# Optimization experiments

Hardware: AMD Instinct MI355X
Metric: run time of the kernel (lower is better)

## Reference

```python
import jax, jax.numpy as jnp
import numpy as np

HEADS = 4
OUT_DIM = 64
NEG_SLOPE = 0.2


def setup_inputs() -> dict:
    key = jax.random.key(0)
    k1, k2, k3, k4 = jax.random.split(key, 4)
    n, in_dim = 4096, 256
    x = jax.random.normal(k1, (n, in_dim), dtype=jnp.float32)
    adj = jax.random.randint(k2, (n, n), 0, 2, dtype=jnp.int32)
    # lin: in_dim -> heads*out_dim (no bias), stored as [in_dim, heads*out_dim]
    W = jax.random.normal(k3, (in_dim, HEADS * OUT_DIM), dtype=jnp.float32) * 0.05
    # att_weight: [heads, 2*out_dim]
    att = jax.random.normal(k4, (HEADS, 2 * OUT_DIM), dtype=jnp.float32) * 0.05
    return {"x": x, "adj": adj, "W": W, "att": att}


def reference(x, adj, W, att):
    n = x.shape[0]
    h = (x @ W).reshape(n, HEADS, OUT_DIM)  # [n, H, D]
    # scores[i,j,h] = att[h] . cat(h_i, h_j) = <h_i, a_src[h]> + <h_j, a_dst[h]>
    a_src, a_dst = att[:, :OUT_DIM], att[:, OUT_DIM:]
    e_src = jnp.einsum('nhd,hd->nh', h, a_src)  # [n, H]
    e_dst = jnp.einsum('nhd,hd->nh', h, a_dst)  # [n, H]
    scores = e_src[:, None, :] + e_dst[None, :, :]  # [n, n, H]
    scores = jax.nn.leaky_relu(scores, negative_slope=NEG_SLOPE)
    mask = (adj > 0)[:, :, None]  # [n, n, 1]
    scores = jnp.where(mask, scores, -jnp.inf)
    alpha = jax.nn.softmax(scores, axis=1)  # softmax over neighbors j
    # h_prime[i,h,d] = sum_j alpha[i,j,h] * h[j,h,d]
    h_prime = jnp.einsum('ijh,jhd->ihd', alpha, h)
    return h_prime.reshape(n, HEADS * OUT_DIM)
```

## Files before the change

kernel.cpp:

```cpp
#include <hip/hip_runtime.h>
#include <hip/hip_bf16.h>

#define HEADS 4
#define ODIM 64
#define HD 256
#define NEG_SLOPE 0.2f

typedef __attribute__((ext_vector_type(8))) short bf16x8;
typedef __attribute__((ext_vector_type(4))) float floatx4;

__global__ __launch_bounds__(256) void pack_x(const float* __restrict__ x,
                                              __hip_bfloat16* __restrict__ xh,
                                              __hip_bfloat16* __restrict__ xl, int K) {
    const int g = blockIdx.x * 256 + threadIdx.x;
    const int lane = g & 63, frag = g >> 6;
    const int Kc = K >> 5;
    const int kc = frag % Kc, mc = frag / Kc;
    const int l16 = lane & 15, q = lane >> 4;
    const float* src = x + (size_t)(mc * 16 + l16) * K + kc * 32 + q * 8;
    const float4 v0 = *(const float4*)src;
    const float4 v1 = *(const float4*)(src + 4);
    const float vv[8] = {v0.x, v0.y, v0.z, v0.w, v1.x, v1.y, v1.z, v1.w};
    union { __hip_bfloat16 b[8]; bf16x8 v; } H, L;
    #pragma unroll
    for (int p = 0; p < 8; ++p) {
        H.b[p] = __float2bfloat16(vv[p]);
        L.b[p] = __float2bfloat16(vv[p] - __bfloat162float(H.b[p]));
    }
    *(bf16x8*)&xh[(size_t)frag * 512 + lane * 8] = H.v;
    *(bf16x8*)&xl[(size_t)frag * 512 + lane * 8] = L.v;
}

__global__ __launch_bounds__(256) void pack_w(const float* __restrict__ W,
                                              __hip_bfloat16* __restrict__ wh,
                                              __hip_bfloat16* __restrict__ wl,
                                              int N, int K) {
    const int g = blockIdx.x * 256 + threadIdx.x;
    const int lane = g & 63, frag = g >> 6;
    const int Kc = K >> 5;
    const int kc = frag % Kc, nc = frag / Kc;
    const int l16 = lane & 15, q = lane >> 4;
    union { __hip_bfloat16 b[8]; bf16x8 v; } H, L;
    #pragma unroll
    for (int p = 0; p < 8; ++p) {
        const float w = W[(size_t)(kc * 32 + q * 8 + p) * N + nc * 16 + l16];
        H.b[p] = __float2bfloat16(w);
        L.b[p] = __float2bfloat16(w - __bfloat162float(H.b[p]));
    }
    *(bf16x8*)&wh[(size_t)frag * 512 + lane * 8] = H.v;
    *(bf16x8*)&wl[(size_t)frag * 512 + lane * 8] = L.v;
}

__global__ __launch_bounds__(256) void gemm_fused(
    const __hip_bfloat16* __restrict__ xh, const __hip_bfloat16* __restrict__ xl,
    const __hip_bfloat16* __restrict__ wh, const __hip_bfloat16* __restrict__ wl,
    const float* __restrict__ att, float4* __restrict__ E4,
    __hip_bfloat16* __restrict__ hbB, int n, int K) {

    __shared__ __hip_bfloat16 T[64][80];

    const int tid = threadIdx.x, wave = tid >> 6, lane = tid & 63;
    const int q = lane >> 4, l16 = lane & 15;
    const int m0 = blockIdx.x * 64;
    const int head = blockIdx.y;
    const int Kc = K >> 5;
    const int mc = (m0 >> 4) + wave;

    floatx4 acc[4] = {{0.f,0.f,0.f,0.f},{0.f,0.f,0.f,0.f},{0.f,0.f,0.f,0.f},{0.f,0.f,0.f,0.f}};

    const __hip_bfloat16* Ab[3] = {xh, xh, xl};
    const __hip_bfloat16* Bb[3] = {wh, wl, wh};
    #pragma unroll
    for (int pass = 0; pass < 3; ++pass) {
        const __hip_bfloat16* A = Ab[pass] + (size_t)mc * Kc * 512 + lane * 8;
        const __hip_bfloat16* B = Bb[pass] + lane * 8;
        for (int kc = 0; kc < Kc; ++kc) {
            const bf16x8 af = *(const bf16x8*)(A + (size_t)kc * 512);
            #pragma unroll
            for (int nt = 0; nt < 4; ++nt) {
                const bf16x8 bf = *(const bf16x8*)(B + (size_t)((head * 4 + nt) * Kc + kc) * 512);
                acc[nt] = __builtin_amdgcn_mfma_f32_16x16x32_bf16(af, bf, acc[nt], 0, 0, 0);
            }
        }
    }

    float as_v[4], ad_v[4];
    #pragma unroll
    for (int nt = 0; nt < 4; ++nt) {
        as_v[nt] = att[head * 2 * ODIM + nt * 16 + l16];
        ad_v[nt] = att[head * 2 * ODIM + ODIM + nt * 16 + l16];
    }
    #pragma unroll
    for (int r = 0; r < 4; ++r) {
        float ps = 0.f, pd = 0.f;
        #pragma unroll
        for (int nt = 0; nt < 4; ++nt) {
            ps = fmaf(acc[nt][r], as_v[nt], ps);
            pd = fmaf(acc[nt][r], ad_v[nt], pd);
        }
        #pragma unroll
        for (int m = 1; m <= 8; m <<= 1) {
            ps += __shfl_xor(ps, m, 64);
            pd += __shfl_xor(pd, m, 64);
        }
        if (l16 == 0) {
            const int i = m0 + wave * 16 + q * 4 + r;
            E4[i * HEADS + head] = make_float4(__expf(ps), __expf(NEG_SLOPE * ps),
                                               __expf(pd), __expf(NEG_SLOPE * pd));
        }
    }

    #pragma unroll
    for (int nt = 0; nt < 4; ++nt) {
        union { __hip_bfloat16 b[4]; uint2 u; } pk;
        #pragma unroll
        for (int r = 0; r < 4; ++r) pk.b[r] = __float2bfloat16(acc[nt][r]);
        *(uint2*)&T[nt * 16 + l16][wave * 16 + q * 4] = pk.u;
    }
    __syncthreads();

    #pragma unroll
    for (int ffi = 0; ffi < 2; ++ffi) {
        const int ff = (tid >> 6) + ffi * 4;
        const int kcl = ff >> 2, nt = ff & 3;
        const bf16x8 v = *(const bf16x8*)&T[nt * 16 + l16][kcl * 32 + q * 8];
        const size_t frag = ((size_t)head * (n >> 5) + (m0 >> 5) + kcl) * 4 + nt;
        *(bf16x8*)&hbB[frag * 512 + lane * 8] = v;
    }
}

__global__ __launch_bounds__(256, 4) void aggregate(
    const int* __restrict__ adj, const float4* __restrict__ E4,
    const __hip_bfloat16* __restrict__ hbB, float* __restrict__ outsp,
    float* __restrict__ densp, int n, int KR) {

    __shared__ unsigned short adjL[32][88];
    __shared__ float2 EdL[HEADS][64];

    const int tid = threadIdx.x;
    const int wave = tid >> 6, lane = tid & 63;
    const int q = lane >> 4, l16 = lane & 15, q8 = (lane >> 4) * 8;
    const int i0 = blockIdx.x * 32;
    const int K0 = blockIdx.y * KR;

    const int sr = tid >> 3, sg = (tid & 7) * 8;
    const int je = tid >> 2, he = tid & 3;

    float es1[2], es2[2];
    #pragma unroll
    for (int mt = 0; mt < 2; ++mt) {
        const float4 e = E4[(i0 + mt * 16 + l16) * HEADS + wave];
        es1[mt] = e.x; es2[mt] = e.y;
    }

    union { short s[8]; bf16x8 v; } bones;
    #pragma unroll
    for (int p = 0; p < 8; ++p) bones.s[p] = (l16 == 0) ? (short)0x3F80 : (short)0;

    floatx4 acc[2][4];
    floatx4 accd[2];
    #pragma unroll
    for (int mt = 0; mt < 2; ++mt) {
        accd[mt] = (floatx4){0.f, 0.f, 0.f, 0.f};
        #pragma unroll
        for (int nt = 0; nt < 4; ++nt) acc[mt][nt] = (floatx4){0.f, 0.f, 0.f, 0.f};
    }

    int4 aj0, aj1; float4 ev;
    {
        const int* ap = &adj[(size_t)(i0 + sr) * n + K0 + sg];
        aj0 = *(const int4*)ap; aj1 = *(const int4*)(ap + 4);
        ev = E4[(K0 + je) * HEADS + he];
    }

    for (int jc = K0; jc < K0 + KR; jc += 64) {
        __syncthreads();
        {
            const int av[8] = {aj0.x, aj0.y, aj0.z, aj0.w, aj1.x, aj1.y, aj1.z, aj1.w};
            uint4 u;
            u.x = (av[0] > 0 ? 0xFFFFu : 0u) | (av[1] > 0 ? 0xFFFF0000u : 0u);
            u.y = (av[2] > 0 ? 0xFFFFu : 0u) | (av[3] > 0 ? 0xFFFF0000u : 0u);
            u.z = (av[4] > 0 ? 0xFFFFu : 0u) | (av[5] > 0 ? 0xFFFF0000u : 0u);
            u.w = (av[6] > 0 ? 0xFFFFu : 0u) | (av[7] > 0 ? 0xFFFF0000u : 0u);
            *(uint4*)&adjL[sr][sg] = u;
            EdL[he][je] = make_float2(ev.z, ev.w);
        }
        __syncthreads();
        {
            int jn = jc + 64; if (jn >= K0 + KR) jn = K0;
            const int* ap = &adj[(size_t)(i0 + sr) * n + jn + sg];
            aj0 = *(const int4*)ap; aj1 = *(const int4*)(ap + 4);
            ev = E4[(jn + je) * HEADS + he];
        }
        bf16x8 bfr[2][4];
        const size_t kbase = (size_t)wave * (n >> 5) + (jc >> 5);
        #pragma unroll
        for (int ks = 0; ks < 2; ++ks)
            #pragma unroll
            for (int nt = 0; nt < 4; ++nt)
                bfr[ks][nt] = *(const bf16x8*)&hbB[((kbase + ks) * 4 + nt) * 512 + lane * 8];

        #pragma unroll
        for (int ks = 0; ks < 2; ++ks) {
            const float4* ep = (const float4*)&EdL[wave][ks * 32 + q8];
            const float4 e0 = ep[0], e1 = ep[1], e2 = ep[2], e3 = ep[3];
            const float edz[8] = {e0.x, e0.z, e1.x, e1.z, e2.x, e2.z, e3.x, e3.z};
            const float edw[8] = {e0.y, e0.w, e1.y, e1.w, e2.y, e2.w, e3.y, e3.w};
            #pragma unroll
            for (int mt = 0; mt < 2; ++mt) {
                const uint4 msk = *(const uint4*)&adjL[mt * 16 + l16][ks * 32 + q8];
                const unsigned int mm[4] = {msk.x, msk.y, msk.z, msk.w};
                union { unsigned int u[4]; bf16x8 v; } af;
                #pragma unroll
                for (int p = 0; p < 4; ++p) {
                    const float wa = fmaxf(es1[mt] * edz[2 * p],     es2[mt] * edw[2 * p]);
                    const float wb = fmaxf(es1[mt] * edz[2 * p + 1], es2[mt] * edw[2 * p + 1]);
                    union { __hip_bfloat16 b[2]; unsigned int u; } pk;
                    pk.b[0] = __float2bfloat16(wa);
                    pk.b[1] = __float2bfloat16(wb);
                    af.u[p] = pk.u & mm[p];
                }
                #pragma unroll
                for (int nt = 0; nt < 4; ++nt)
                    acc[mt][nt] = __builtin_amdgcn_mfma_f32_16x16x32_bf16(af.v, bfr[ks][nt], acc[mt][nt], 0, 0, 0);
                accd[mt] = __builtin_amdgcn_mfma_f32_16x16x32_bf16(af.v, bones.v, accd[mt], 0, 0, 0);
            }
        }
    }

    const size_t sOut = (size_t)blockIdx.y * n * HD;
    #pragma unroll
    for (int mt = 0; mt < 2; ++mt)
        #pragma unroll
        for (int nt = 0; nt < 4; ++nt)
            #pragma unroll
            for (int r = 0; r < 4; ++r)
                outsp[sOut + (size_t)(i0 + mt * 16 + q * 4 + r) * HD + wave * ODIM + nt * 16 + l16] = acc[mt][nt][r];
    if (l16 == 0) {
        #pragma unroll
        for (int mt = 0; mt < 2; ++mt)
            #pragma unroll
            for (int r = 0; r < 4; ++r)
                densp[((size_t)blockIdx.y * n + i0 + mt * 16 + q * 4 + r) * HEADS + wave] = accd[mt][r];
    }
}

__global__ __launch_bounds__(256) void normalize(const float* __restrict__ outsp,
                                                 const float* __restrict__ densp,
                                                 float* __restrict__ out, int n, int splits) {
    const int g = blockIdx.x * 256 + threadIdx.x;
    const int i = g >> 6;
    const int c4 = (g & 63) * 4;
    const int head = c4 >> 6;
    float den = 0.f;
    for (int s = 0; s < splits; ++s) den += densp[((size_t)s * n + i) * HEADS + head];
    float4 v = {0.f, 0.f, 0.f, 0.f};
    for (int s = 0; s < splits; ++s) {
        const float4 t = *(const float4*)&outsp[(size_t)s * n * HD + (size_t)i * HD + c4];
        v.x += t.x; v.y += t.y; v.z += t.z; v.w += t.w;
    }
    const float inv = 1.0f / den;
    v.x *= inv; v.y *= inv; v.z *= inv; v.w *= inv;
    *(float4*)&out[(size_t)i * HD + c4] = v;
}

extern "C" void kernel_launch(void* const* d_in, const int* in_sizes, int n_in,
                              void* d_out, int out_size, void* d_ws, size_t ws_size,
                              hipStream_t stream) {
    const float* x   = (const float*)d_in[0];
    const int*   adj = (const int*)d_in[1];
    const float* W   = (const float*)d_in[2];
    const float* att = (const float*)d_in[3];
    float* out = (float*)d_out;

    const int in_dim = in_sizes[2] / HD;
    const int n = in_sizes[0] / in_dim;

    char* ws = (char*)d_ws;
    size_t off = 0;
    auto alloc = [&](size_t bytes) -> void* {
        void* p = ws + off; off += (bytes + 255) & ~(size_t)255; return p;
    };
    __hip_bfloat16* xh = (__hip_bfloat16*)alloc((size_t)n * in_dim * 2);
    __hip_bfloat16* xl = (__hip_bfloat16*)alloc((size_t)n * in_dim * 2);
    __hip_bfloat16* wh = (__hip_bfloat16*)alloc((size_t)in_dim * HD * 2);
    __hip_bfloat16* wl = (__hip_bfloat16*)alloc((size_t)in_dim * HD * 2);
    float4*         E4 = (float4*)alloc((size_t)n * HEADS * 16);
    __hip_bfloat16* hbB = (__hip_bfloat16*)alloc((size_t)n * HD * 2);

    const size_t outB = (size_t)n * HD * 4, denB = (size_t)n * HEADS * 4;
    int splits = 1;
    if      (ws_size >= off + 8 * (outB + denB)) splits = 8;
    else if (ws_size >= off + 4 * (outB + denB)) splits = 4;
    else if (ws_size >= off + 2 * (outB + denB)) splits = 2;
    float* densp = (float*)alloc((size_t)splits * denB);
    float* outsp = (splits == 1) ? out : (float*)alloc((size_t)splits * outB);

    pack_x<<<(n / 16) * (in_dim / 32) * 64 / 256, 256, 0, stream>>>(x, xh, xl, in_dim);
    pack_w<<<(HD / 16) * (in_dim / 32) * 64 / 256, 256, 0, stream>>>(W, wh, wl, HD, in_dim);
    gemm_fused<<<dim3(n / 64, HEADS), 256, 0, stream>>>(xh, xl, wh, wl, att, E4, hbB, n, in_dim);
    aggregate<<<dim3(n / 32, splits), 256, 0, stream>>>(adj, E4, hbB, outsp, densp, n, n / splits);
    normalize<<<n * 64 / 256, 256, 0, stream>>>(outsp, densp, out, n, splits);
}
```

Baseline: 147.4 us.

## Merge pack kernels, fuse GEMM passes, double-buffer aggregate LDS staging

Merges the x and W packing kernels into a single launch to save one kernel launch. Folds the three split-bf16 GEMM passes into one K loop, so each A fragment is loaded once and feeds three MFMAs. In aggregate, the adjacency-mask and E_dst LDS tiles are double-buffered, cutting the barriers per iteration from two to one. It also uses packed float2 multiplies and a byte-perm to truncate floats to bf16. The perm truncates instead of rounding to nearest, which slightly changes numerics.

```diff
diff --git a/kernel.cpp b/kernel.cpp
--- a/kernel.cpp
+++ b/kernel.cpp
@@ -8,47 +8,49 @@
 
 typedef __attribute__((ext_vector_type(8))) short bf16x8;
 typedef __attribute__((ext_vector_type(4))) float floatx4;
-
-__global__ __launch_bounds__(256) void pack_x(const float* __restrict__ x,
-                                              __hip_bfloat16* __restrict__ xh,
-                                              __hip_bfloat16* __restrict__ xl, int K) {
-    const int g = blockIdx.x * 256 + threadIdx.x;
-    const int lane = g & 63, frag = g >> 6;
+typedef __attribute__((ext_vector_type(2))) float floatx2;
+
+__global__ __launch_bounds__(256) void pack_xw(const float* __restrict__ x,
+                                               const float* __restrict__ W,
+                                               __hip_bfloat16* __restrict__ xh,
+                                               __hip_bfloat16* __restrict__ xl,
+                                               __hip_bfloat16* __restrict__ wh,
+                                               __hip_bfloat16* __restrict__ wl,
+                                               int K, int nxb) {
+    const int b = blockIdx.x;
     const int Kc = K >> 5;
-    const int kc = frag % Kc, mc = frag / Kc;
-    const int l16 = lane & 15, q = lane >> 4;
-    const float* src = x + (size_t)(mc * 16 + l16) * K + kc * 32 + q * 8;
-    const float4 v0 = *(const float4*)src;
-    const float4 v1 = *(const float4*)(src + 4);
-    const float vv[8] = {v0.x, v0.y, v0.z, v0.w, v1.x, v1.y, v1.z, v1.w};
-    union { __hip_bfloat16 b[8]; bf16x8 v; } H, L;
-    #pragma unroll
-    for (int p = 0; p < 8; ++p) {
-        H.b[p] = __float2bfloat16(vv[p]);
-        L.b[p] = __float2bfloat16(vv[p] - __bfloat162float(H.b[p]));
-    }
-    *(bf16x8*)&xh[(size_t)frag * 512 + lane * 8] = H.v;
-    *(bf16x8*)&xl[(size_t)frag * 512 + lane * 8] = L.v;
-}
-
-__global__ __launch_bounds__(256) void pack_w(const float* __restrict__ W,
-                                              __hip_bfloat16* __restrict__ wh,
-                                              __hip_bfloat16* __restrict__ wl,
-                                              int N, int K) {
-    const int g = blockIdx.x * 256 + threadIdx.x;
-    const int lane = g & 63, frag = g >> 6;
-    const int Kc = K >> 5;
-    const int kc = frag % Kc, nc = frag / Kc;
-    const int l16 = lane & 15, q = lane >> 4;
-    union { __hip_bfloat16 b[8]; bf16x8 v; } H, L;
-    #pragma unroll
-    for (int p = 0; p < 8; ++p) {
-        const float w = W[(size_t)(kc * 32 + q * 8 + p) * N + nc * 16 + l16];
-        H.b[p] = __float2bfloat16(w);
-        L.b[p] = __float2bfloat16(w - __bfloat162float(H.b[p]));
-    }
-    *(bf16x8*)&wh[(size_t)frag * 512 + lane * 8] = H.v;
-    *(bf16x8*)&wl[(size_t)frag * 512 + lane * 8] = L.v;
+    if (b < nxb) {
+        const int g = b * 256 + threadIdx.x;
+        const int lane = g & 63, frag = g >> 6;
+        const int kc = frag % Kc, mc = frag / Kc;
+        const int l16 = lane & 15, q = lane >> 4;
+        const float* src = x + (size_t)(mc * 16 + l16) * K + kc * 32 + q * 8;
+        const float4 v0 = *(const float4*)src;
+        const float4 v1 = *(const float4*)(src + 4);
+        const float vv[8] = {v0.x, v0.y, v0.z, v0.w, v1.x, v1.y, v1.z, v1.w};
+        union { __hip_bfloat16 b[8]; bf16x8 v; } H, L;
+        #pragma unroll
+        for (int p = 0; p < 8; ++p) {
+            H.b[p] = __float2bfloat16(vv[p]);
+            L.b[p] = __float2bfloat16(vv[p] - __bfloat162float(H.b[p]));
+        }
+        *(bf16x8*)&xh[(size_t)frag * 512 + lane * 8] = H.v;
+        *(bf16x8*)&xl[(size_t)frag * 512 + lane * 8] = L.v;
+    } else {
+        const int g = (b - nxb) * 256 + threadIdx.x;
+        const int lane = g & 63, frag = g >> 6;
+        const int kc = frag % Kc, nc = frag / Kc;
+        const int l16 = lane & 15, q = lane >> 4;
+        union { __hip_bfloat16 b[8]; bf16x8 v; } H, L;
+        #pragma unroll
+        for (int p = 0; p < 8; ++p) {
+            const float w = W[(size_t)(kc * 32 + q * 8 + p) * HD + nc * 16 + l16];
+            H.b[p] = __float2bfloat16(w);
+            L.b[p] = __float2bfloat16(w - __bfloat162float(H.b[p]));
+        }
+        *(bf16x8*)&wh[(size_t)frag * 512 + lane * 8] = H.v;
+        *(bf16x8*)&wl[(size_t)frag * 512 + lane * 8] = L.v;
+    }
 }
 
 __global__ __launch_bounds__(256) void gemm_fused(
@@ -68,19 +70,22 @@
 
     floatx4 acc[4] = {{0.f,0.f,0.f,0.f},{0.f,0.f,0.f,0.f},{0.f,0.f,0.f,0.f},{0.f,0.f,0.f,0.f}};
 
-    const __hip_bfloat16* Ab[3] = {xh, xh, xl};
-    const __hip_bfloat16* Bb[3] = {wh, wl, wh};
-    #pragma unroll
-    for (int pass = 0; pass < 3; ++pass) {
-        const __hip_bfloat16* A = Ab[pass] + (size_t)mc * Kc * 512 + lane * 8;
-        const __hip_bfloat16* B = Bb[pass] + lane * 8;
-        for (int kc = 0; kc < Kc; ++kc) {
-            const bf16x8 af = *(const bf16x8*)(A + (size_t)kc * 512);
-            #pragma unroll
-            for (int nt = 0; nt < 4; ++nt) {
-                const bf16x8 bf = *(const bf16x8*)(B + (size_t)((head * 4 + nt) * Kc + kc) * 512);
-                acc[nt] = __builtin_amdgcn_mfma_f32_16x16x32_bf16(af, bf, acc[nt], 0, 0, 0);
-            }
+    const __hip_bfloat16* Axh = xh + (size_t)mc * Kc * 512 + lane * 8;
+    const __hip_bfloat16* Axl = xl + (size_t)mc * Kc * 512 + lane * 8;
+    const __hip_bfloat16* Bwh = wh + lane * 8;
+    const __hip_bfloat16* Bwl = wl + lane * 8;
+    #pragma unroll 2
+    for (int kc = 0; kc < Kc; ++kc) {
+        const bf16x8 ah = *(const bf16x8*)(Axh + (size_t)kc * 512);
+        const bf16x8 al = *(const bf16x8*)(Axl + (size_t)kc * 512);
+        #pragma unroll
+        for (int nt = 0; nt < 4; ++nt) {
+            const size_t fo = (size_t)((head * 4 + nt) * Kc + kc) * 512;
+            const bf16x8 bh = *(const bf16x8*)(Bwh + fo);
+            const bf16x8 bl = *(const bf16x8*)(Bwl + fo);
+            acc[nt] = __builtin_amdgcn_mfma_f32_16x16x32_bf16(ah, bh, acc[nt], 0, 0, 0);
+            acc[nt] = __builtin_amdgcn_mfma_f32_16x16x32_bf16(ah, bl, acc[nt], 0, 0, 0);
+            acc[nt] = __builtin_amdgcn_mfma_f32_16x16x32_bf16(al, bh, acc[nt], 0, 0, 0);
         }
     }
 
@@ -134,8 +139,8 @@
     const __hip_bfloat16* __restrict__ hbB, float* __restrict__ outsp,
     float* __restrict__ densp, int n, int KR) {
 
-    __shared__ unsigned short adjL[32][88];
-    __shared__ float2 EdL[HEADS][64];
+    __shared__ unsigned short adjL[2][32][72];
+    __shared__ float2 EdL[2][HEADS][64];
 
     const int tid = threadIdx.x;
     const int wave = tid >> 6, lane = tid & 63;
@@ -146,11 +151,11 @@
     const int sr = tid >> 3, sg = (tid & 7) * 8;
     const int je = tid >> 2, he = tid & 3;
 
-    float es1[2], es2[2];
+    floatx2 es12[2];
     #pragma unroll
     for (int mt = 0; mt < 2; ++mt) {
         const float4 e = E4[(i0 + mt * 16 + l16) * HEADS + wave];
-        es1[mt] = e.x; es2[mt] = e.y;
+        es12[mt][0] = e.x; es12[mt][1] = e.y;
     }
 
     union { short s[8]; bf16x8 v; } bones;
@@ -166,66 +171,76 @@
         for (int nt = 0; nt < 4; ++nt) acc[mt][nt] = (floatx4){0.f, 0.f, 0.f, 0.f};
     }
 
+    const int* aprow = &adj[(size_t)(i0 + sr) * n];
+
     int4 aj0, aj1; float4 ev;
     {
-        const int* ap = &adj[(size_t)(i0 + sr) * n + K0 + sg];
+        const int* ap = aprow + K0 + sg;
         aj0 = *(const int4*)ap; aj1 = *(const int4*)(ap + 4);
         ev = E4[(K0 + je) * HEADS + he];
     }
-
+    auto stage = [&](int buf) {
+        const int av[8] = {aj0.x, aj0.y, aj0.z, aj0.w, aj1.x, aj1.y, aj1.z, aj1.w};
+        uint4 u;
+        u.x = (av[0] > 0 ? 0xFFFFu : 0u) | (av[1] > 0 ? 0xFFFF0000u : 0u);
+        u.y = (av[2] > 0 ? 0xFFFFu : 0u) | (av[3] > 0 ? 0xFFFF0000u : 0u);
+        u.z = (av[4] > 0 ? 0xFFFFu : 0u) | (av[5] > 0 ? 0xFFFF0000u : 0u);
+        u.w = (av[6] > 0 ? 0xFFFFu : 0u) | (av[7] > 0 ? 0xFFFF0000u : 0u);
+        *(uint4*)&adjL[buf][sr][sg] = u;
+        EdL[buf][he][je] = make_float2(ev.z, ev.w);
+    };
+    stage(0);
+    __syncthreads();
+
+    int cur = 0;
     for (int jc = K0; jc < K0 + KR; jc += 64) {
-        __syncthreads();
+        int jn = jc + 64; if (jn >= K0 + KR) jn = K0;
         {
-            const int av[8] = {aj0.x, aj0.y, aj0.z, aj0.w, aj1.x, aj1.y, aj1.z, aj1.w};
-            uint4 u;
-            u.x = (av[0] > 0 ? 0xFFFFu : 0u) | (av[1] > 0 ? 0xFFFF0000u : 0u);
-            u.y = (av[2] > 0 ? 0xFFFFu : 0u) | (av[3] > 0 ? 0xFFFF0000u : 0u);
-            u.z = (av[4] > 0 ? 0xFFFFu : 0u) | (av[5] > 0 ? 0xFFFF0000u : 0u);
-            u.w = (av[6] > 0 ? 0xFFFFu : 0u) | (av[7] > 0 ? 0xFFFF0000u : 0u);
-            *(uint4*)&adjL[sr][sg] = u;
-            EdL[he][je] = make_float2(ev.z, ev.w);
-        }
-        __syncthreads();
-        {
-            int jn = jc + 64; if (jn >= K0 + KR) jn = K0;
-            const int* ap = &adj[(size_t)(i0 + sr) * n + jn + sg];
+            const int* ap = aprow + jn + sg;
             aj0 = *(const int4*)ap; aj1 = *(const int4*)(ap + 4);
             ev = E4[(jn + je) * HEADS + he];
         }
-        bf16x8 bfr[2][4];
-        const size_t kbase = (size_t)wave * (n >> 5) + (jc >> 5);
-        #pragma unroll
-        for (int ks = 0; ks < 2; ++ks)
+
+        const size_t kbase = ((size_t)wave * (n >> 5) + (jc >> 5)) * 4;
+        #pragma unroll
+        for (int ks = 0; ks < 2; ++ks) {
+            bf16x8 bfr[4];
             #pragma unroll
             for (int nt = 0; nt < 4; ++nt)
-                bfr[ks][nt] = *(const bf16x8*)&hbB[((kbase + ks) * 4 + nt) * 512 + lane * 8];
-
-        #pragma unroll
-        for (int ks = 0; ks < 2; ++ks) {
-            const float4* ep = (const float4*)&EdL[wave][ks * 32 + q8];
-            const float4 e0 = ep[0], e1 = ep[1], e2 = ep[2], e3 = ep[3];
-            const float edz[8] = {e0.x, e0.z, e1.x, e1.z, e2.x, e2.z, e3.x, e3.z};
-            const float edw[8] = {e0.y, e0.w, e1.y, e1.w, e2.y, e2.w, e3.y, e3.w};
+                bfr[nt] = *(const bf16x8*)&hbB[(kbase + ks * 4 + nt) * 512 + lane * 8];
+
+            const float4* ep = (const float4*)&EdL[cur][wave][ks * 32 + q8];
+            const float4 e01 = ep[0], e23 = ep[1], e45 = ep[2], e67 = ep[3];
+            floatx2 ed[8];
+            ed[0][0]=e01.x; ed[0][1]=e01.y;  ed[1][0]=e01.z; ed[1][1]=e01.w;
+            ed[2][0]=e23.x; ed[2][1]=e23.y;  ed[3][0]=e23.z; ed[3][1]=e23.w;
+            ed[4][0]=e45.x; ed[4][1]=e45.y;  ed[5][0]=e45.z; ed[5][1]=e45.w;
+            ed[6][0]=e67.x; ed[6][1]=e67.y;  ed[7][0]=e67.z; ed[7][1]=e67.w;
+
             #pragma unroll
             for (int mt = 0; mt < 2; ++mt) {
-                const uint4 msk = *(const uint4*)&adjL[mt * 16 + l16][ks * 32 + q8];
+                const uint4 msk = *(const uint4*)&adjL[cur][mt * 16 + l16][ks * 32 + q8];
                 const unsigned int mm[4] = {msk.x, msk.y, msk.z, msk.w};
                 union { unsigned int u[4]; bf16x8 v; } af;
                 #pragma unroll
                 for (int p = 0; p < 4; ++p) {
-                    const float wa = fmaxf(es1[mt] * edz[2 * p],     es2[mt] * edw[2 * p]);
-                    const float wb = fmaxf(es1[mt] * edz[2 * p + 1], es2[mt] * edw[2 * p + 1]);
-                    union { __hip_bfloat16 b[2]; unsigned int u; } pk;
-                    pk.b[0] = __float2bfloat16(wa);
-                    pk.b[1] = __float2bfloat16(wb);
-                    af.u[p] = pk.u & mm[p];
+                    const floatx2 pa = es12[mt] * ed[2 * p];
+                    const floatx2 pb = es12[mt] * ed[2 * p + 1];
+                    const float wa = fmaxf(pa[0], pa[1]);
+                    const float wb = fmaxf(pb[0], pb[1]);
+                    af.u[p] = __builtin_amdgcn_perm(__float_as_uint(wb), __float_as_uint(wa),
+                                                    0x07060302u) & mm[p];
                 }
                 #pragma unroll
                 for (int nt = 0; nt < 4; ++nt)
-                    acc[mt][nt] = __builtin_amdgcn_mfma_f32_16x16x32_bf16(af.v, bfr[ks][nt], acc[mt][nt], 0, 0, 0);
+                    acc[mt][nt] = __builtin_amdgcn_mfma_f32_16x16x32_bf16(af.v, bfr[nt], acc[mt][nt], 0, 0, 0);
                 accd[mt] = __builtin_amdgcn_mfma_f32_16x16x32_bf16(af.v, bones.v, accd[mt], 0, 0, 0);
             }
         }
+
+        stage(cur ^ 1);
+        __syncthreads();
+        cur ^= 1;
     }
 
     const size_t sOut = (size_t)blockIdx.y * n * HD;
@@ -296,8 +311,9 @@
     float* densp = (float*)alloc((size_t)splits * denB);
     float* outsp = (splits == 1) ? out : (float*)alloc((size_t)splits * outB);
 
-    pack_x<<<(n / 16) * (in_dim / 32) * 64 / 256, 256, 0, stream>>>(x, xh, xl, in_dim);
-    pack_w<<<(HD / 16) * (in_dim / 32) * 64 / 256, 256, 0, stream>>>(W, wh, wl, HD, in_dim);
+    const int nxb = (n / 16) * (in_dim / 32) * 64 / 256;
+    const int nwb = (HD / 16) * (in_dim / 32) * 64 / 256;
+    pack_xw<<<nxb + nwb, 256, 0, stream>>>(x, W, xh, xl, wh, wl, in_dim, nxb);
     gemm_fused<<<dim3(n / 64, HEADS), 256, 0, stream>>>(xh, xl, wh, wl, att, E4, hbB, n, in_dim);
     aggregate<<<dim3(n / 32, splits), 256, 0, stream>>>(adj, E4, hbB, outsp, densp, n, n / splits);
     normalize<<<n * 64 / 256, 256, 0, stream>>>(outsp, densp, out, n, splits);
```

Result: no change. 147.4 us (-0.0%).
